# Kernel optimization log

Hardware: AMD Instinct MI355X
Metric: run time of the kernel (lower is better)

The kernel has to match this reference:

```python
import jax, jax.numpy as jnp
import numpy as np

NEG_SLOPE = 0.2


def gatv2_layer(x, edge_index, Wl, Wr, att, bias):
    """PyG GATv2Conv (share_weights=False, concat=True, negative_slope=0.2).
    x: [N, F]; Wl/Wr: [F, H*C]; att: [H, C]; bias: [H*C]. Returns [N, H*C]."""
    N = x.shape[0]
    H, C = att.shape
    src, dst = edge_index[0], edge_index[1]
    xl = (x @ Wl).reshape(N, H, C)  # source transform
    xr = (x @ Wr).reshape(N, H, C)  # target transform
    # per-edge attention logits
    e = jax.nn.leaky_relu(xl[src] + xr[dst], NEG_SLOPE)          # [E, H, C]
    logits = jnp.einsum('ehc,hc->eh', e, att)                     # [E, H]
    # segment softmax over incoming edges of each destination node
    m = jax.ops.segment_max(logits, dst, num_segments=N)          # [N, H]
    m = jnp.where(jnp.isfinite(m), m, 0.0)                        # empty segments
    ex = jnp.exp(logits - m[dst])                                 # [E, H]
    denom = jax.ops.segment_sum(ex, dst, num_segments=N)          # [N, H]
    alpha = ex / (denom[dst] + 1e-16)                             # [E, H]
    msg = xl[src] * alpha[..., None]                              # [E, H, C]
    out = jax.ops.segment_sum(msg, dst, num_segments=N)           # [N, H, C]
    return out.reshape(N, H * C) + bias


def setup_inputs() -> dict:
    key = jax.random.key(0)
    ks = jax.random.split(key, 10)
    N, E, F, H, C, OUT = 50000, 800000, 256, 8, 32, 64
    s = 0.05
    return {
        'x': jax.random.normal(ks[0], (N, F), dtype=jnp.float32),
        'edge_index': jax.random.randint(ks[1], (2, E), 0, N, dtype=jnp.int64),
        'Wl1': jax.random.normal(ks[2], (F, H * C), dtype=jnp.float32) * s,
        'Wr1': jax.random.normal(ks[3], (F, H * C), dtype=jnp.float32) * s,
        'att1': jax.random.normal(ks[4], (H, C), dtype=jnp.float32) * s,
        'b1': jax.random.normal(ks[5], (H * C,), dtype=jnp.float32) * s,
        'Wl2': jax.random.normal(ks[6], (H * C, OUT), dtype=jnp.float32) * s,
        'Wr2': jax.random.normal(ks[7], (H * C, OUT), dtype=jnp.float32) * s,
        'att2': jax.random.normal(ks[8], (1, OUT), dtype=jnp.float32) * s,
        'b2': jax.random.normal(ks[9], (OUT,), dtype=jnp.float32) * s,
    }


def reference(x, edge_index, Wl1, Wr1, att1, b1, Wl2, Wr2, att2, b2):
    h = gatv2_layer(x, edge_index, Wl1, Wr1, att1, b1)
    h = jax.nn.relu(h)
    h = gatv2_layer(h, edge_index, Wl2, Wr2, att2, b2)
    return (h, jax.nn.log_softmax(h, axis=1))
```

## Files before the change

### kernel.cpp

```cpp
#include <hip/hip_runtime.h>
#include <hip/hip_bf16.h>
#include <math.h>

#define NEG_SLOPE 0.2f

typedef __attribute__((ext_vector_type(8))) short short8;
typedef __attribute__((ext_vector_type(4))) float floatx4;
typedef __attribute__((ext_vector_type(2))) float floatx2;

__device__ inline ushort f2b(float f) {
    __hip_bfloat16 b = __float2bfloat16(f);
    return *(ushort*)&b;
}
__device__ inline floatx2 bf2x2(unsigned int d) {
    union { unsigned int i; float f; } lo, hi;
    lo.i = d << 16;
    hi.i = d & 0xffff0000u;
    floatx2 r = {lo.f, hi.f};
    return r;
}

template<int BM, int BN>
__global__ __launch_bounds__(256) void gemm_bf16(const ushort* __restrict__ A,
                                                 const ushort* __restrict__ Bt,
                                                 ushort* __restrict__ C,
                                                 int M, int N, int K)
{
    constexpr int SA = 40;
    constexpr int WTM = (BN == 64) ? 32 : 64;
    constexpr int WM  = BM / WTM;
    constexpr int IT  = WTM / 16;
    constexpr int JT  = 4;
    __shared__ ushort As[BM * SA];
    __shared__ ushort Bs[BN * SA];
    const int tid = threadIdx.x;
    const int w = tid >> 6, lane = tid & 63;
    const int mw = (w % WM) * WTM;
    const int nw = (w / WM) * 64;
    const int m0 = blockIdx.y * BM;
    const int n0 = blockIdx.x * BN;
    const int lm = lane & 15;
    const int kg = lane >> 4;

    floatx4 acc[IT][JT];
#pragma unroll
    for (int i = 0; i < IT; ++i)
#pragma unroll
        for (int j = 0; j < JT; ++j) acc[i][j] = (floatx4)0.f;

    for (int k0 = 0; k0 < K; k0 += 32) {
#pragma unroll
        for (int it = 0; it < BM / 64; ++it) {
            int idx = it * 256 + tid;
            int row = idx >> 2, kc = idx & 3;
            int grow = m0 + row;
            if (grow >= M) grow = M - 1;
            short8 v = *(const short8*)&A[(size_t)grow * K + k0 + kc * 8];
            *(short8*)&As[row * SA + kc * 8] = v;
        }
#pragma unroll
        for (int it = 0; it < BN / 64; ++it) {
            int idx = it * 256 + tid;
            int row = idx >> 2, kc = idx & 3;
            short8 v = *(const short8*)&Bt[(size_t)(n0 + row) * K + k0 + kc * 8];
            *(short8*)&Bs[row * SA + kc * 8] = v;
        }
        __syncthreads();
        short8 a[IT], b[JT];
#pragma unroll
        for (int i = 0; i < IT; ++i)
            a[i] = *(const short8*)&As[(mw + i * 16 + lm) * SA + kg * 8];
#pragma unroll
        for (int j = 0; j < JT; ++j)
            b[j] = *(const short8*)&Bs[(nw + j * 16 + lm) * SA + kg * 8];
#pragma unroll
        for (int i = 0; i < IT; ++i)
#pragma unroll
            for (int j = 0; j < JT; ++j)
                acc[i][j] = __builtin_amdgcn_mfma_f32_16x16x32_bf16(a[i], b[j], acc[i][j], 0, 0, 0);
        __syncthreads();
    }

#pragma unroll
    for (int i = 0; i < IT; ++i) {
        int rbase = m0 + mw + i * 16 + (lane >> 4) * 4;
#pragma unroll
        for (int j = 0; j < JT; ++j) {
            int col = n0 + nw + j * 16 + lm;
#pragma unroll
            for (int r = 0; r < 4; ++r) {
                int row = rbase + r;
                if (row < M) C[(size_t)row * N + col] = f2b(acc[i][j][r]);
            }
        }
    }
}

__global__ void k_prep(const float* __restrict__ x, ushort* __restrict__ xb, int XB,
                       const float* __restrict__ Wl1, const float* __restrict__ Wr1,
                       const float* __restrict__ Wl2, const float* __restrict__ Wr2,
                       ushort* __restrict__ wlr1t, ushort* __restrict__ wlr2t,
                       const int* __restrict__ dst, int E, int* __restrict__ counts)
{
    const int b = blockIdx.x;
    const int t = threadIdx.x;
    if (b < XB) {
        int i = b * 2048 + t * 8;
        float4 f0 = *(const float4*)&x[i];
        float4 f1 = *(const float4*)&x[i + 4];
        short8 o;
        o[0] = (short)f2b(f0.x); o[1] = (short)f2b(f0.y);
        o[2] = (short)f2b(f0.z); o[3] = (short)f2b(f0.w);
        o[4] = (short)f2b(f1.x); o[5] = (short)f2b(f1.y);
        o[6] = (short)f2b(f1.z); o[7] = (short)f2b(f1.w);
        *(short8*)&xb[i] = o;
    } else if (b < XB + 640) {
        int i = (b - XB) * 256 + t;
        if (i < 65536) {
            int k = i >> 8, n = i & 255;
            wlr1t[n * 256 + k] = f2b(Wl1[i]);
        } else if (i < 131072) {
            int j = i - 65536;
            int k = j >> 8, n = j & 255;
            wlr1t[65536 + n * 256 + k] = f2b(Wr1[j]);
        } else if (i < 147456) {
            int j = i - 131072;
            int k = j >> 6, n = j & 63;
            wlr2t[n * 256 + k] = f2b(Wl2[j]);
        } else {
            int j = i - 147456;
            int k = j >> 6, n = j & 63;
            wlr2t[16384 + n * 256 + k] = f2b(Wr2[j]);
        }
    } else {
        int i = (b - XB - 640) * 256 + t;
        if (i < E) atomicAdd(&counts[dst[i]], 1);
    }
}

__global__ void k_chunksum(const int* __restrict__ counts, int N, int* __restrict__ chunk)
{
    __shared__ int sm[256];
    const int t = threadIdx.x;
    const int base = blockIdx.x * 1024;
    int s = 0;
    for (int i = t; i < 1024; i += 256) {
        int idx = base + i;
        s += (idx < N) ? counts[idx] : 0;
    }
    sm[t] = s;
    __syncthreads();
    for (int off = 128; off; off >>= 1) {
        if (t < off) sm[t] += sm[t + off];
        __syncthreads();
    }
    if (t == 0) chunk[blockIdx.x] = sm[0];
}

__global__ void k_scanchunk(int* __restrict__ chunk, int nchunks)
{
    const int t = threadIdx.x;
    int v = (t < nchunks) ? chunk[t] : 0;
    int inc = v;
#pragma unroll
    for (int off = 1; off < 64; off <<= 1) {
        int y = __shfl_up(inc, off);
        if (t >= off) inc += y;
    }
    if (t < nchunks) chunk[t] = inc - v;
    if (t == nchunks - 1) chunk[nchunks] = inc;
}

__global__ void k_scanwrite(const int* __restrict__ counts, int N,
                            const int* __restrict__ chunk,
                            int* __restrict__ offsets, int* __restrict__ cursor)
{
    __shared__ int sm[256];
    const int t = threadIdx.x;
    const int base = blockIdx.x * 1024 + t * 4;
    int v[4];
    int s = 0;
#pragma unroll
    for (int i = 0; i < 4; ++i) {
        v[i] = (base + i < N) ? counts[base + i] : 0;
        s += v[i];
    }
    sm[t] = s;
    __syncthreads();
    for (int off = 1; off < 256; off <<= 1) {
        int y = (t >= off) ? sm[t - off] : 0;
        __syncthreads();
        sm[t] += y;
        __syncthreads();
    }
    int run = chunk[blockIdx.x] + sm[t] - s;
#pragma unroll
    for (int i = 0; i < 4; ++i) {
        if (base + i < N) {
            offsets[base + i] = run;
            cursor[base + i] = run;
        }
        run += v[i];
    }
    if (blockIdx.x == 0 && t == 0) offsets[N] = chunk[gridDim.x];
}

__global__ void k_fill(const int* __restrict__ src, const int* __restrict__ dst,
                       int E, int* __restrict__ cursor, int* __restrict__ csr_off)
{
    int i = blockIdx.x * blockDim.x + threadIdx.x;
    if (i < E) {
        int d = dst[i];
        int pos = atomicAdd(&cursor[d], 1);
        csr_off[pos] = src[i] * 1024;
    }
}

__global__ __launch_bounds__(256) void agg1(const ushort* __restrict__ xlr,
                                            const float* __restrict__ att,
                                            const float* __restrict__ bias,
                                            const int* __restrict__ offsets,
                                            const int* __restrict__ csr_off,
                                            ushort* __restrict__ h1, int N)
{
    const int wave = blockIdx.x * 4 + (threadIdx.x >> 6);
    const int lane = threadIdx.x & 63;
    if (wave >= N) return;
    const int n = wave;
    const int g = lane >> 5;
    const int sl = lane & 31;
    const int elem = (sl >> 2) * 32 + (sl & 3) * 8;
    const char* __restrict__ xbase = (const char*)xlr;
    const int ebyte = elem * 2;

    floatx2 attv2[4], xrv2[4];
    {
        uint4 xr8 = *(const uint4*)(xbase + (size_t)n * 1024 + 512 + ebyte);
        unsigned int xw[4] = {xr8.x, xr8.y, xr8.z, xr8.w};
#pragma unroll
        for (int i = 0; i < 4; ++i) {
            attv2[i] = *(const floatx2*)&att[elem + 2 * i];
            xrv2[i] = bf2x2(xw[i]);
        }
    }
    float m = -1e30f, l = 0.f;
    floatx2 acc2[4] = {(floatx2)0.f, (floatx2)0.f, (floatx2)0.f, (floatx2)0.f};

    const int beg = offsets[n], end = offsets[n + 1];
    uint4 vA, vB;
    int oC;
    {
        int k0 = beg + g;
        if (k0 < end) vA = *(const uint4*)(xbase + (unsigned)csr_off[k0] + ebyte);
        if (k0 + 2 < end) vB = *(const uint4*)(xbase + (unsigned)csr_off[k0 + 2] + ebyte);
        if (k0 + 4 < end) oC = csr_off[k0 + 4];
    }
    for (int kk = beg + g; kk < end; kk += 2) {
        uint4 cur = vA;
        vA = vB;
        if (kk + 4 < end) vB = *(const uint4*)(xbase + (unsigned)oC + ebyte);
        if (kk + 6 < end) oC = csr_off[kk + 6];

        unsigned int cw[4] = {cur.x, cur.y, cur.z, cur.w};
        floatx2 xl2[4];
        floatx2 u2 = (floatx2)0.f;
#pragma unroll
        for (int i = 0; i < 4; ++i) {
            xl2[i] = bf2x2(cw[i]);
            floatx2 t = xl2[i] + xrv2[i];
            t = __builtin_elementwise_max(t, t * NEG_SLOPE);
            u2 += t * attv2[i];
        }
        float u = u2.x + u2.y;
        u += __shfl_xor(u, 1);
        u += __shfl_xor(u, 2);
        float e = __expf(-fabsf(u - m));
        bool kp = (m >= u);
        float sc = kp ? 1.f : e;
        float p  = kp ? e : 1.f;
        m = fmaxf(m, u);
#pragma unroll
        for (int i = 0; i < 4; ++i) acc2[i] = acc2[i] * sc + xl2[i] * p;
        l = fmaf(l, sc, p);
    }
    {
        float mo = __shfl_xor(m, 32);
        float lo = __shfl_xor(l, 32);
        float nm = fmaxf(m, mo);
        float ea = __expf(m - nm);
        float eb = __expf(mo - nm);
#pragma unroll
        for (int i = 0; i < 4; ++i) {
            floatx2 ao = {__shfl_xor(acc2[i].x, 32), __shfl_xor(acc2[i].y, 32)};
            acc2[i] = acc2[i] * ea + ao * eb;
        }
        l = l * ea + lo * eb;
    }
    if (g == 0) {
        float rl = 1.f / (l + 1e-16f);
        short8 o;
#pragma unroll
        for (int i = 0; i < 4; ++i) {
            float v0 = fmaf(acc2[i].x, rl, bias[elem + 2 * i]);
            float v1 = fmaf(acc2[i].y, rl, bias[elem + 2 * i + 1]);
            o[2 * i]     = (short)f2b(fmaxf(v0, 0.f));
            o[2 * i + 1] = (short)f2b(fmaxf(v1, 0.f));
        }
        *(short8*)&h1[(size_t)n * 256 + elem] = o;
    }
}

__global__ __launch_bounds__(256) void agg2(const ushort* __restrict__ xlr,
                                            const float* __restrict__ att,
                                            const float* __restrict__ bias,
                                            const int* __restrict__ offsets,
                                            const int* __restrict__ csr_off,
                                            float* __restrict__ out, int N)
{
    const int wave = blockIdx.x * 4 + (threadIdx.x >> 6);
    const int lane = threadIdx.x & 63;
    if (wave >= N) return;
    const int n = wave;
    const int g = lane >> 4;
    const int c0 = (lane & 15) * 4;
    const char* __restrict__ xbase = (const char*)xlr;
    const int cbyte = c0 * 2;

    floatx2 attv2[2], xrv2[2];
    {
        uint2 xr4 = *(const uint2*)(xbase + (size_t)n * 256 + 128 + cbyte);
        attv2[0] = *(const floatx2*)&att[c0];
        attv2[1] = *(const floatx2*)&att[c0 + 2];
        xrv2[0] = bf2x2(xr4.x);
        xrv2[1] = bf2x2(xr4.y);
    }
    float m = -1e30f, l = 0.f;
    floatx2 acc2[2] = {(floatx2)0.f, (floatx2)0.f};

    const int beg = offsets[n], end = offsets[n + 1];
    uint2 vA, vB;
    int oC;
    {
        int k0 = beg + g;
        if (k0 < end) vA = *(const uint2*)(xbase + ((unsigned)csr_off[k0] >> 2) + cbyte);
        if (k0 + 4 < end) vB = *(const uint2*)(xbase + ((unsigned)csr_off[k0 + 4] >> 2) + cbyte);
        if (k0 + 8 < end) oC = csr_off[k0 + 8];
    }
    for (int kk = beg + g; kk < end; kk += 4) {
        uint2 cur = vA;
        vA = vB;
        if (kk + 8 < end) vB = *(const uint2*)(xbase + ((unsigned)oC >> 2) + cbyte);
        if (kk + 12 < end) oC = csr_off[kk + 12];

        floatx2 xl2[2];
        xl2[0] = bf2x2(cur.x);
        xl2[1] = bf2x2(cur.y);
        floatx2 u2 = (floatx2)0.f;
#pragma unroll
        for (int i = 0; i < 2; ++i) {
            floatx2 t = xl2[i] + xrv2[i];
            t = __builtin_elementwise_max(t, t * NEG_SLOPE);
            u2 += t * attv2[i];
        }
        float u = u2.x + u2.y;
        u += __shfl_xor(u, 1);
        u += __shfl_xor(u, 2);
        u += __shfl_xor(u, 4);
        u += __shfl_xor(u, 8);
        float e = __expf(-fabsf(u - m));
        bool kp = (m >= u);
        float sc = kp ? 1.f : e;
        float p  = kp ? e : 1.f;
        m = fmaxf(m, u);
#pragma unroll
        for (int i = 0; i < 2; ++i) acc2[i] = acc2[i] * sc + xl2[i] * p;
        l = fmaf(l, sc, p);
    }
#pragma unroll
    for (int off = 16; off <= 32; off <<= 1) {
        float mo = __shfl_xor(m, off);
        float lo = __shfl_xor(l, off);
        float nm = fmaxf(m, mo);
        float sa = __expf(m - nm);
        float sb = __expf(mo - nm);
#pragma unroll
        for (int i = 0; i < 2; ++i) {
            floatx2 ao = {__shfl_xor(acc2[i].x, off), __shfl_xor(acc2[i].y, off)};
            acc2[i] = acc2[i] * sa + ao * sb;
        }
        l = l * sa + lo * sb;
        m = nm;
    }
    float rl = 1.f / (l + 1e-16f);
    float h[4];
    h[0] = acc2[0].x * rl + bias[c0];
    h[1] = acc2[0].y * rl + bias[c0 + 1];
    h[2] = acc2[1].x * rl + bias[c0 + 2];
    h[3] = acc2[1].y * rl + bias[c0 + 3];

    float mx = fmaxf(fmaxf(h[0], h[1]), fmaxf(h[2], h[3]));
    mx = fmaxf(mx, __shfl_xor(mx, 1));
    mx = fmaxf(mx, __shfl_xor(mx, 2));
    mx = fmaxf(mx, __shfl_xor(mx, 4));
    mx = fmaxf(mx, __shfl_xor(mx, 8));
    float ssum = __expf(h[0] - mx) + __expf(h[1] - mx) + __expf(h[2] - mx) + __expf(h[3] - mx);
    ssum += __shfl_xor(ssum, 1);
    ssum += __shfl_xor(ssum, 2);
    ssum += __shfl_xor(ssum, 4);
    ssum += __shfl_xor(ssum, 8);
    float lg = __logf(ssum);
    if (g == 0) {
        float4 o1 = make_float4(h[0], h[1], h[2], h[3]);
        *(float4*)&out[(size_t)n * 64 + c0] = o1;
        float4 o2 = make_float4(h[0] - mx - lg, h[1] - mx - lg, h[2] - mx - lg, h[3] - mx - lg);
        *(float4*)&out[(size_t)(N + n) * 64 + c0] = o2;
    }
}

extern "C" void kernel_launch(void* const* d_in, const int* in_sizes, int n_in,
                              void* d_out, int out_size, void* d_ws, size_t ws_size,
                              hipStream_t stream)
{
    const float* x    = (const float*)d_in[0];
    const int*   ei   = (const int*)d_in[1];
    const float* Wl1  = (const float*)d_in[2];
    const float* Wr1  = (const float*)d_in[3];
    const float* att1 = (const float*)d_in[4];
    const float* b1   = (const float*)d_in[5];
    const float* Wl2  = (const float*)d_in[6];
    const float* Wr2  = (const float*)d_in[7];
    const float* att2 = (const float*)d_in[8];
    const float* b2   = (const float*)d_in[9];
    float* out = (float*)d_out;

    const int F = 256;
    const int E = in_sizes[1] / 2;
    const int N = in_sizes[0] / F;

    const int* e_src = ei;
    const int* e_dst = ei + E;

    ushort* xb    = (ushort*)d_ws;
    ushort* wlr1t = xb + (size_t)N * 256;
    ushort* wlr2t = wlr1t + 512 * 256;
    ushort* xlr1  = wlr2t + 128 * 256;
    ushort* h1b   = xlr1 + (size_t)N * 512;
    ushort* xlr2  = h1b + (size_t)N * 256;
    int* offsets  = (int*)(xlr2 + (size_t)N * 128);
    int* cursor   = offsets + (N + 1);
    int* counts   = cursor + (N + 1);
    int* chunkoff = counts + N;
    int* csr_off  = chunkoff + 66;

    const int nchunks = (N + 1023) / 1024;
    const int XB = (N * 256) / 2048;

    hipMemsetAsync(counts, 0, (size_t)N * sizeof(int), stream);
    k_prep<<<XB + 640 + (E + 255) / 256, 256, 0, stream>>>(
        x, xb, XB, Wl1, Wr1, Wl2, Wr2, wlr1t, wlr2t, e_dst, E, counts);

    gemm_bf16<128, 128><<<dim3(4, (N + 127) / 128), 256, 0, stream>>>(xb, wlr1t, xlr1, N, 512, F);

    k_chunksum<<<nchunks, 256, 0, stream>>>(counts, N, chunkoff);
    k_scanchunk<<<1, 64, 0, stream>>>(chunkoff, nchunks);
    k_scanwrite<<<nchunks, 256, 0, stream>>>(counts, N, chunkoff, offsets, cursor);
    k_fill<<<(E + 255) / 256, 256, 0, stream>>>(e_src, e_dst, E, cursor, csr_off);

    agg1<<<(N + 3) / 4, 256, 0, stream>>>(xlr1, att1, b1, offsets, csr_off, h1b, N);

    gemm_bf16<128, 64><<<dim3(2, (N + 127) / 128), 256, 0, stream>>>(h1b, wlr2t, xlr2, N, 128, 256);
    agg2<<<(N + 3) / 4, 256, 0, stream>>>(xlr2, att2, b2, offsets, csr_off, out, N);
}
```

Before: 340.5 us.

## Use direct global-to-LDS loads in GEMM and widen agg2 edge parallelism

The GEMM tile loads now use global_load_lds to write 16-byte chunks straight into unpadded shared memory instead of staging through registers. The aim is to cut VGPR traffic and load instructions, at the risk of LDS bank conflicts now that the padding is gone. The CSR array gets 16 zero-padded tail entries so the agg1 and agg2 prefetch loads can drop their bounds checks. agg2 is reorganised so each lane handles 8 channels with 16-byte loads and a wave covers 8 edges per step, cutting shuffle rounds and per-edge overhead, with only one level of prefetch.

```diff
diff --git a/kernel.cpp b/kernel.cpp
--- a/kernel.cpp
+++ b/kernel.cpp
@@ -20,19 +20,23 @@
     return r;
 }
 
+#define GLOAD_LDS16(gp, lp)                                                    \
+    __builtin_amdgcn_global_load_lds(                                          \
+        (const __attribute__((address_space(1))) unsigned int*)(gp),           \
+        (__attribute__((address_space(3))) unsigned int*)(lp), 16, 0, 0)
+
 template<int BM, int BN>
 __global__ __launch_bounds__(256) void gemm_bf16(const ushort* __restrict__ A,
                                                  const ushort* __restrict__ Bt,
                                                  ushort* __restrict__ C,
                                                  int M, int N, int K)
 {
-    constexpr int SA = 40;
     constexpr int WTM = (BN == 64) ? 32 : 64;
     constexpr int WM  = BM / WTM;
     constexpr int IT  = WTM / 16;
     constexpr int JT  = 4;
-    __shared__ ushort As[BM * SA];
-    __shared__ ushort Bs[BN * SA];
+    __shared__ ushort As[BM * 32];
+    __shared__ ushort Bs[BN * 32];
     const int tid = threadIdx.x;
     const int w = tid >> 6, lane = tid & 63;
     const int mw = (w % WM) * WTM;
@@ -42,6 +46,8 @@
     const int lm = lane & 15;
     const int kg = lane >> 4;
 
+    const int srow = tid >> 2, skc = tid & 3;
+
     floatx4 acc[IT][JT];
 #pragma unroll
     for (int i = 0; i < IT; ++i)
@@ -51,28 +57,26 @@
     for (int k0 = 0; k0 < K; k0 += 32) {
 #pragma unroll
         for (int it = 0; it < BM / 64; ++it) {
-            int idx = it * 256 + tid;
-            int row = idx >> 2, kc = idx & 3;
+            int row = it * 64 + srow;
             int grow = m0 + row;
             if (grow >= M) grow = M - 1;
-            short8 v = *(const short8*)&A[(size_t)grow * K + k0 + kc * 8];
-            *(short8*)&As[row * SA + kc * 8] = v;
+            GLOAD_LDS16(&A[(size_t)grow * K + k0 + skc * 8],
+                        As + (it * 256 + w * 64) * 8);
         }
 #pragma unroll
         for (int it = 0; it < BN / 64; ++it) {
-            int idx = it * 256 + tid;
-            int row = idx >> 2, kc = idx & 3;
-            short8 v = *(const short8*)&Bt[(size_t)(n0 + row) * K + k0 + kc * 8];
-            *(short8*)&Bs[row * SA + kc * 8] = v;
+            int row = it * 64 + srow;
+            GLOAD_LDS16(&Bt[(size_t)(n0 + row) * K + k0 + skc * 8],
+                        Bs + (it * 256 + w * 64) * 8);
         }
         __syncthreads();
         short8 a[IT], b[JT];
 #pragma unroll
         for (int i = 0; i < IT; ++i)
-            a[i] = *(const short8*)&As[(mw + i * 16 + lm) * SA + kg * 8];
+            a[i] = *(const short8*)&As[(mw + i * 16 + lm) * 32 + kg * 8];
 #pragma unroll
         for (int j = 0; j < JT; ++j)
-            b[j] = *(const short8*)&Bs[(nw + j * 16 + lm) * SA + kg * 8];
+            b[j] = *(const short8*)&Bs[(nw + j * 16 + lm) * 32 + kg * 8];
 #pragma unroll
         for (int i = 0; i < IT; ++i)
 #pragma unroll
@@ -214,6 +218,7 @@
         int pos = atomicAdd(&cursor[d], 1);
         csr_off[pos] = src[i] * 1024;
     }
+    if (i < 16) csr_off[E + i] = 0;
 }
 
 __global__ __launch_bounds__(256) void agg1(const ushort* __restrict__ xlr,
@@ -251,15 +256,15 @@
     int oC;
     {
         int k0 = beg + g;
-        if (k0 < end) vA = *(const uint4*)(xbase + (unsigned)csr_off[k0] + ebyte);
-        if (k0 + 2 < end) vB = *(const uint4*)(xbase + (unsigned)csr_off[k0 + 2] + ebyte);
-        if (k0 + 4 < end) oC = csr_off[k0 + 4];
+        vA = *(const uint4*)(xbase + (unsigned)csr_off[k0] + ebyte);
+        vB = *(const uint4*)(xbase + (unsigned)csr_off[k0 + 2] + ebyte);
+        oC = csr_off[k0 + 4];
     }
     for (int kk = beg + g; kk < end; kk += 2) {
         uint4 cur = vA;
         vA = vB;
-        if (kk + 4 < end) vB = *(const uint4*)(xbase + (unsigned)oC + ebyte);
-        if (kk + 6 < end) oC = csr_off[kk + 6];
+        vB = *(const uint4*)(xbase + (unsigned)oC + ebyte);
+        oC = csr_off[kk + 6];
 
         unsigned int cw[4] = {cur.x, cur.y, cur.z, cur.w};
         floatx2 xl2[4];
@@ -321,43 +326,43 @@
     const int lane = threadIdx.x & 63;
     if (wave >= N) return;
     const int n = wave;
-    const int g = lane >> 4;
-    const int c0 = (lane & 15) * 4;
+    const int g = lane >> 3;
+    const int cl = lane & 7;
     const char* __restrict__ xbase = (const char*)xlr;
-    const int cbyte = c0 * 2;
-
-    floatx2 attv2[2], xrv2[2];
+    const int cbyte = cl * 16;
+
+    floatx2 attv2[4], xrv2[4];
     {
-        uint2 xr4 = *(const uint2*)(xbase + (size_t)n * 256 + 128 + cbyte);
-        attv2[0] = *(const floatx2*)&att[c0];
-        attv2[1] = *(const floatx2*)&att[c0 + 2];
-        xrv2[0] = bf2x2(xr4.x);
-        xrv2[1] = bf2x2(xr4.y);
+        uint4 xr8 = *(const uint4*)(xbase + (size_t)n * 256 + 128 + cbyte);
+        unsigned int xw[4] = {xr8.x, xr8.y, xr8.z, xr8.w};
+#pragma unroll
+        for (int i = 0; i < 4; ++i) {
+            attv2[i] = *(const floatx2*)&att[cl * 8 + 2 * i];
+            xrv2[i] = bf2x2(xw[i]);
+        }
     }
     float m = -1e30f, l = 0.f;
-    floatx2 acc2[2] = {(floatx2)0.f, (floatx2)0.f};
+    floatx2 acc2[4] = {(floatx2)0.f, (floatx2)0.f, (floatx2)0.f, (floatx2)0.f};
 
     const int beg = offsets[n], end = offsets[n + 1];
-    uint2 vA, vB;
-    int oC;
+    uint4 vA;
+    int oB;
     {
         int k0 = beg + g;
-        if (k0 < end) vA = *(const uint2*)(xbase + ((unsigned)csr_off[k0] >> 2) + cbyte);
-        if (k0 + 4 < end) vB = *(const uint2*)(xbase + ((unsigned)csr_off[k0 + 4] >> 2) + cbyte);
-        if (k0 + 8 < end) oC = csr_off[k0 + 8];
-    }
-    for (int kk = beg + g; kk < end; kk += 4) {
-        uint2 cur = vA;
-        vA = vB;
-        if (kk + 8 < end) vB = *(const uint2*)(xbase + ((unsigned)oC >> 2) + cbyte);
-        if (kk + 12 < end) oC = csr_off[kk + 12];
-
-        floatx2 xl2[2];
-        xl2[0] = bf2x2(cur.x);
-        xl2[1] = bf2x2(cur.y);
+        vA = *(const uint4*)(xbase + ((unsigned)csr_off[k0] >> 2) + cbyte);
+        oB = csr_off[k0 + 8];
+    }
+    for (int kk = beg + g; kk < end; kk += 8) {
+        uint4 cur = vA;
+        vA = *(const uint4*)(xbase + ((unsigned)oB >> 2) + cbyte);
+        oB = csr_off[kk + 16];
+
+        unsigned int cw[4] = {cur.x, cur.y, cur.z, cur.w};
+        floatx2 xl2[4];
         floatx2 u2 = (floatx2)0.f;
 #pragma unroll
-        for (int i = 0; i < 2; ++i) {
+        for (int i = 0; i < 4; ++i) {
+            xl2[i] = bf2x2(cw[i]);
             floatx2 t = xl2[i] + xrv2[i];
             t = __builtin_elementwise_max(t, t * NEG_SLOPE);
             u2 += t * attv2[i];
@@ -366,25 +371,24 @@
         u += __shfl_xor(u, 1);
         u += __shfl_xor(u, 2);
         u += __shfl_xor(u, 4);
-        u += __shfl_xor(u, 8);
         float e = __expf(-fabsf(u - m));
         bool kp = (m >= u);
         float sc = kp ? 1.f : e;
         float p  = kp ? e : 1.f;
         m = fmaxf(m, u);
 #pragma unroll
-        for (int i = 0; i < 2; ++i) acc2[i] = acc2[i] * sc + xl2[i] * p;
+        for (int i = 0; i < 4; ++i) acc2[i] = acc2[i] * sc + xl2[i] * p;
         l = fmaf(l, sc, p);
     }
 #pragma unroll
-    for (int off = 16; off <= 32; off <<= 1) {
+    for (int off = 8; off <= 32; off <<= 1) {
         float mo = __shfl_xor(m, off);
         float lo = __shfl_xor(l, off);
         float nm = fmaxf(m, mo);
         float sa = __expf(m - nm);
         float sb = __expf(mo - nm);
 #pragma unroll
-        for (int i = 0; i < 2; ++i) {
+        for (int i = 0; i < 4; ++i) {
             floatx2 ao = {__shfl_xor(acc2[i].x, off), __shfl_xor(acc2[i].y, off)};
             acc2[i] = acc2[i] * sa + ao * sb;
         }
@@ -392,28 +396,35 @@
         m = nm;
     }
     float rl = 1.f / (l + 1e-16f);
-    float h[4];
-    h[0] = acc2[0].x * rl + bias[c0];
-    h[1] = acc2[0].y * rl + bias[c0 + 1];
-    h[2] = acc2[1].x * rl + bias[c0 + 2];
-    h[3] = acc2[1].y * rl + bias[c0 + 3];
-
-    float mx = fmaxf(fmaxf(h[0], h[1]), fmaxf(h[2], h[3]));
+    float h[8];
+#pragma unroll
+    for (int i = 0; i < 4; ++i) {
+        h[2 * i]     = fmaf(acc2[i].x, rl, bias[cl * 8 + 2 * i]);
+        h[2 * i + 1] = fmaf(acc2[i].y, rl, bias[cl * 8 + 2 * i + 1]);
+    }
+
+    float mx = h[0];
+#pragma unroll
+    for (int i = 1; i < 8; ++i) mx = fmaxf(mx, h[i]);
     mx = fmaxf(mx, __shfl_xor(mx, 1));
     mx = fmaxf(mx, __shfl_xor(mx, 2));
     mx = fmaxf(mx, __shfl_xor(mx, 4));
-    mx = fmaxf(mx, __shfl_xor(mx, 8));
-    float ssum = __expf(h[0] - mx) + __expf(h[1] - mx) + __expf(h[2] - mx) + __expf(h[3] - mx);
+    float ssum = 0.f;
+#pragma unroll
+    for (int i = 0; i < 8; ++i) ssum += __expf(h[i] - mx);
     ssum += __shfl_xor(ssum, 1);
     ssum += __shfl_xor(ssum, 2);
     ssum += __shfl_xor(ssum, 4);
-    ssum += __shfl_xor(ssum, 8);
-    float lg = __logf(ssum);
+    float lg = mx + __logf(ssum);
     if (g == 0) {
-        float4 o1 = make_float4(h[0], h[1], h[2], h[3]);
-        *(float4*)&out[(size_t)n * 64 + c0] = o1;
-        float4 o2 = make_float4(h[0] - mx - lg, h[1] - mx - lg, h[2] - mx - lg, h[3] - mx - lg);
-        *(float4*)&out[(size_t)(N + n) * 64 + c0] = o2;
+        float4 o0 = make_float4(h[0], h[1], h[2], h[3]);
+        float4 o1 = make_float4(h[4], h[5], h[6], h[7]);
+        *(float4*)&out[(size_t)n * 64 + cl * 8] = o0;
+        *(float4*)&out[(size_t)n * 64 + cl * 8 + 4] = o1;
+        float4 s0 = make_float4(h[0] - lg, h[1] - lg, h[2] - lg, h[3] - lg);
+        float4 s1 = make_float4(h[4] - lg, h[5] - lg, h[6] - lg, h[7] - lg);
+        *(float4*)&out[(size_t)(N + n) * 64 + cl * 8] = s0;
+        *(float4*)&out[(size_t)(N + n) * 64 + cl * 8 + 4] = s1;
     }
 }
 
```

After: 345.4 us. About the same (+1.4%).
